# Optimization experiments

Hardware: AMD Instinct MI355X
Metric: run time of the kernel (lower is better)

## Reference

```python
import jax, jax.numpy as jnp
import numpy as np

NSTATES = 16
NCOM = 4
NHIDDEN = 256
BATCH = 262144


def _orthogonal(key, out_dim, in_dim):
    # mimic torch.nn.init.orthogonal_
    big, small = max(out_dim, in_dim), min(out_dim, in_dim)
    a = jax.random.normal(key, (big, small), dtype=jnp.float32)
    q, r = jnp.linalg.qr(a)
    q = q * jnp.sign(jnp.diagonal(r))  # make deterministic / uniform
    if out_dim < in_dim:
        q = q.T
    return q


def setup_inputs() -> dict:
    key = jax.random.key(0)
    k0, k1, k2, k3, k4 = jax.random.split(key, 5)
    zstates = jax.random.normal(k0, (BATCH, NSTATES), dtype=jnp.float32)
    W1 = _orthogonal(k1, NHIDDEN, NSTATES)            # lin1.weight [nhidden, nstates]
    W2 = _orthogonal(k2, NHIDDEN, NHIDDEN)            # lin2.weight
    W3 = _orthogonal(k3, NHIDDEN, NHIDDEN)            # lin3.weight
    W4 = _orthogonal(k4, NSTATES + NCOM, NHIDDEN)     # lin4.weight [nstates+ncom, nhidden]
    return {"zstates": zstates, "W1": W1, "W2": W2, "W3": W3, "W4": W4}


def _mlp(x, W1, W2, W3, W4):
    # torch Linear (no bias): y = x @ W.T
    h = jax.nn.log_sigmoid(x @ W1.T)
    h = h + jax.nn.log_sigmoid(h @ W2.T)
    h = h + jax.nn.log_sigmoid(h @ W3.T)
    return h @ W4.T


def reference(zstates, W1, W2, W3, W4):
    nstates = NSTATES

    def _get_com_dstates(s):  # s: [nstates]
        nnout = _mlp(s, W1, W2, W3, W4)
        dstates = nnout[:nstates]
        com = nnout[nstates:]
        return com, (dstates, com)

    jac_fcn = jax.vmap(jax.jacrev(_get_com_dstates, argnums=0, has_aux=True))
    dcom_jac, (dstates, com) = jac_fcn(zstates)   # dcom_jac: [B, ncom, nstates]
    # [B, nstates, ncom] concat dstates column -> [B, nstates, ncom+1]
    dcom_jac_t = jnp.swapaxes(dcom_jac, -2, -1)
    mat = jnp.concatenate([dcom_jac_t, dstates[..., None]], axis=-1)
    q, r = jnp.linalg.qr(mat)                     # reduced QR: q [B, nstates, ncom+1]
    dstates_ortho = q[..., -1] * r[..., -1, -1:]  # [B, nstates]
    return dstates_ortho
```

## Files before the change

### kernel.cpp

```cpp
#include <hip/hip_runtime.h>
#include <math.h>

#define NS 16
#define NC 4
#define NH 256
#define BATCH 262144
#define EPB 64
#define HSTR 264

typedef _Float16 half8 __attribute__((ext_vector_type(8)));
typedef _Float16 half4v __attribute__((ext_vector_type(4)));
typedef _Float16 half2v __attribute__((ext_vector_type(2)));
typedef float f32x4 __attribute__((ext_vector_type(4)));

#define MFMA16(a, b, c) __builtin_amdgcn_mfma_f32_16x16x32_f16((a), (b), (c), 0, 0, 0)

#define OFF_W2HI   0
#define OFF_W2LO   65536
#define OFF_W3HI   131072
#define OFF_W3LO   196608
#define OFF_W2THI  262144
#define OFF_W2TLO  327680
#define OFF_W3THI  393216
#define OFF_W3TLO  458752
#define OFF_W1PHI  524288
#define OFF_W1PLO  532480
#define OFF_W1THI  540672
#define OFF_W1TLO  544768
#define OFF_W4HI   548864
#define OFF_W4LO   552960
#define WS_HALVES  557056

__device__ __forceinline__ float logsigf(float a) {
    return fminf(a, 0.f) - __logf(1.f + __expf(-fabsf(a)));
}
__device__ __forceinline__ float siggf(float a) {
    return 1.f / (1.f + __expf(a));
}
__device__ __forceinline__ void split2(float x, _Float16& h, _Float16& l) {
    h = (_Float16)x;
    l = (_Float16)(x - (float)h);
}
__device__ __forceinline__ float wsum16(float v) {
    v += __shfl_xor(v, 1, 64);
    v += __shfl_xor(v, 2, 64);
    v += __shfl_xor(v, 4, 64);
    v += __shfl_xor(v, 8, 64);
    return v;
}
__device__ __forceinline__ unsigned h2u(half2v h) {
    union { half2v h; unsigned u; } c; c.h = h; return c.u;
}
__device__ __forceinline__ half2v u2h(unsigned u) {
    union { half2v h; unsigned u; } c; c.u = u; return c.h;
}
__device__ __forceinline__ uint2 packg(const float g[4]) {
    half2v a, b;
    a[0] = (_Float16)g[0]; a[1] = (_Float16)g[1];
    b[0] = (_Float16)g[2]; b[1] = (_Float16)g[3];
    return make_uint2(h2u(a), h2u(b));
}

extern "C" __global__ void __launch_bounds__(256)
prep_big(const float* __restrict__ W2, const float* __restrict__ W3,
         _Float16* __restrict__ ws) {
    const int mat = blockIdx.y;
    const float* W = mat ? W3 : W2;
    _Float16* Whi  = ws + (mat ? OFF_W3HI  : OFF_W2HI);
    _Float16* Wlo  = Whi + 65536;
    _Float16* WThi = ws + (mat ? OFF_W3THI : OFF_W2THI);
    _Float16* WTlo = WThi + 65536;
    const int r = blockIdx.x, c = threadIdx.x;
    float x = W[r * NH + c];
    _Float16 h, l; split2(x, h, l);
    Whi[r * NH + c] = h;  Wlo[r * NH + c] = l;
    WThi[c * NH + r] = h; WTlo[c * NH + r] = l;
}

extern "C" __global__ void __launch_bounds__(256)
prep_small(const float* __restrict__ W1, const float* __restrict__ W4,
           _Float16* __restrict__ ws) {
    _Float16* W1phi = ws + OFF_W1PHI;
    _Float16* W1plo = ws + OFF_W1PLO;
    _Float16* W1Thi = ws + OFF_W1THI;
    _Float16* W1Tlo = ws + OFF_W1TLO;
    _Float16* W4hi  = ws + OFF_W4HI;
    _Float16* W4lo  = ws + OFF_W4LO;
    const int t = threadIdx.x;
    #pragma unroll
    for (int s = 0; s < NS; s++) {
        float x = W1[t * NS + s];
        _Float16 h, l; split2(x, h, l);
        W1phi[t * 32 + s] = h;        W1plo[t * 32 + s] = l;
        W1phi[t * 32 + 16 + s] = (_Float16)0.f;
        W1plo[t * 32 + 16 + s] = (_Float16)0.f;
        W1Thi[s * NH + t] = h;        W1Tlo[s * NH + t] = l;
    }
    #pragma unroll
    for (int q = 0; q < 16; q++) {
        int idx = q * 256 + t;
        float x = W4[idx];
        _Float16 h, l; split2(x, h, l);
        W4hi[idx] = h; W4lo[idx] = l;
    }
}


__device__ __forceinline__ void gemm_fwd1(const _Float16* __restrict__ Ahi,
                                          const _Float16* U,
                                          int w, int lo16, int hi4, f32x4 acc[2][4]) {
    #pragma unroll
    for (int ks = 0; ks < 8; ks++) {
        half8 bh[4];
        #pragma unroll
        for (int n = 0; n < 4; n++)
            bh[n] = *(const half8*)&U[(16 * n + lo16) * HSTR + ks * 32 + hi4 * 8];
        #pragma unroll
        for (int m = 0; m < 2; m++) {
            int woff = (32 * w + 16 * m + lo16) * NH + ks * 32 + hi4 * 8;
            half8 ah = *(const half8*)&Ahi[woff];
            #pragma unroll
            for (int n = 0; n < 4; n++)
                acc[m][n] = MFMA16(ah, bh[n], acc[m][n]);
        }
    }
}

__device__ __forceinline__ void gemm_bwd1(const _Float16* __restrict__ Ahi,
                                          const _Float16* U,
                                          int w, int lo16, int hi4, f32x4 acc[2][8]) {
    #pragma unroll
    for (int ks = 0; ks < 8; ks++) {
        half8 bh[8];
        #pragma unroll
        for (int n = 0; n < 8; n++)
            bh[n] = *(const half8*)&U[(16 * n + lo16) * HSTR + ks * 32 + hi4 * 8];
        #pragma unroll
        for (int m = 0; m < 2; m++) {
            int woff = (32 * w + 16 * m + lo16) * NH + ks * 32 + hi4 * 8;
            half8 ah = *(const half8*)&Ahi[woff];
            #pragma unroll
            for (int n = 0; n < 8; n++)
                acc[m][n] = MFMA16(ah, bh[n], acc[m][n]);
        }
    }
}

__global__ void __launch_bounds__(512, 1)
comet_mfma(const float* __restrict__ Z,
           const float* __restrict__ W4,
           const _Float16* __restrict__ ws,
           float* __restrict__ OUT)
{
    const _Float16* W2hi  = ws + OFF_W2HI;
    const _Float16* W3hi  = ws + OFF_W3HI;
    const _Float16* W2Thi = ws + OFF_W2THI;
    const _Float16* W3Thi = ws + OFF_W3THI;
    const _Float16* W1phi = ws + OFF_W1PHI;
    const _Float16* W1plo = ws + OFF_W1PLO;
    const _Float16* W1Thi = ws + OFF_W1THI;
    const _Float16* W4hi  = ws + OFF_W4HI;
    const _Float16* W4lo  = ws + OFF_W4LO;

    __shared__ __align__(16) _Float16 U[128 * HSTR];
    __shared__ __align__(16) float Jfin[16 * 260];
    __shared__ __align__(16) float Pb[8 * 272];

    const int tid  = threadIdx.x;
    const int l    = tid & 63, w = tid >> 6;
    const int lo16 = l & 15, hi4 = l >> 4;
    const int ebase = blockIdx.x * EPB;
    const int c4 = lo16 & 3;

    float4 vreg[2];
    #pragma unroll
    for (int m = 0; m < 2; m++)
        vreg[m] = *(const float4*)&W4[(NS + c4) * NH + 32 * w + 16 * m + 4 * hi4];

    uint2 g1u[2][4], g2u[2][4], g3u[2][4];

    {
        f32x4 acc[2][4];
        #pragma unroll
        for (int m = 0; m < 2; m++)
            #pragma unroll
            for (int n = 0; n < 4; n++) acc[m][n] = (f32x4)(0.f);
        half8 bh[4], bl[4];
        #pragma unroll
        for (int n = 0; n < 4; n++) {
            if (hi4 < 2) {
                const float* zp = &Z[(size_t)(ebase + 16 * n + lo16) * NS + hi4 * 8];
                float4 z0 = *(const float4*)zp;
                float4 z1 = *(const float4*)(zp + 4);
                float zz[8] = {z0.x, z0.y, z0.z, z0.w, z1.x, z1.y, z1.z, z1.w};
                #pragma unroll
                for (int r = 0; r < 8; r++) {
                    _Float16 h, lo; split2(zz[r], h, lo);
                    bh[n][r] = h; bl[n][r] = lo;
                }
            } else {
                #pragma unroll
                for (int r = 0; r < 8; r++) { bh[n][r] = (_Float16)0.f; bl[n][r] = (_Float16)0.f; }
            }
        }
        #pragma unroll
        for (int m = 0; m < 2; m++) {
            int woff = (32 * w + 16 * m + lo16) * 32 + hi4 * 8;
            half8 ah = *(const half8*)&W1phi[woff];
            half8 al = *(const half8*)&W1plo[woff];
            #pragma unroll
            for (int n = 0; n < 4; n++) {
                acc[m][n] = MFMA16(ah, bh[n], acc[m][n]);
                acc[m][n] = MFMA16(al, bh[n], acc[m][n]);
                acc[m][n] = MFMA16(ah, bl[n], acc[m][n]);
            }
        }
        #pragma unroll
        for (int m = 0; m < 2; m++)
            #pragma unroll
            for (int n = 0; n < 4; n++) {
                int hoff = (16 * n + lo16) * HSTR + 32 * w + 16 * m + 4 * hi4;
                float gv[4];
                half4v nh, nl;
                #pragma unroll
                for (int r = 0; r < 4; r++) {
                    float a = acc[m][n][r];
                    gv[r] = siggf(a);
                    float hv = logsigf(a);
                    _Float16 xh, xl; split2(hv, xh, xl);
                    nh[r] = xh; nl[r] = xl;
                }
                g1u[m][n] = packg(gv);
                *(half4v*)&U[hoff] = nh;
                *(half4v*)&U[64 * HSTR + hoff] = nl;
            }
    }
    __syncthreads();

    #pragma unroll
    for (int L = 0; L < 2; L++) {
        f32x4 acc[2][4];
        #pragma unroll
        for (int m = 0; m < 2; m++)
            #pragma unroll
            for (int n = 0; n < 4; n++) acc[m][n] = (f32x4)(0.f);
        gemm_fwd1(L ? W3hi : W2hi, U, w, lo16, hi4, acc);
        __syncthreads();
        #pragma unroll
        for (int m = 0; m < 2; m++)
            #pragma unroll
            for (int n = 0; n < 4; n++) {
                int hoff = (16 * n + lo16) * HSTR + 32 * w + 16 * m + 4 * hi4;
                half4v oh = *(const half4v*)&U[hoff];
                half4v ol = *(const half4v*)&U[64 * HSTR + hoff];
                float gv[4];
                half4v nh, nl;
                #pragma unroll
                for (int r = 0; r < 4; r++) {
                    float a = acc[m][n][r];
                    gv[r] = siggf(a);
                    float hv = (float)oh[r] + (float)ol[r] + logsigf(a);
                    _Float16 xh, xl; split2(hv, xh, xl);
                    nh[r] = xh; nl[r] = xl;
                }
                if (L) g3u[m][n] = packg(gv); else g2u[m][n] = packg(gv);
                *(half4v*)&U[hoff] = nh;
                *(half4v*)&U[64 * HSTR + hoff] = nl;
            }
        __syncthreads();
    }

    {
        const int et = w & 3, kh = w >> 2;
        f32x4 acc = (f32x4)(0.f);
        #pragma unroll
        for (int i = 0; i < 4; i++) {
            int ks = 4 * kh + i;
            int boff = (16 * et + lo16) * HSTR + ks * 32 + hi4 * 8;
            half8 bh = *(const half8*)&U[boff];
            half8 bl = *(const half8*)&U[64 * HSTR + boff];
            int woff = lo16 * NH + ks * 32 + hi4 * 8;
            half8 ah = *(const half8*)&W4hi[woff];
            half8 al = *(const half8*)&W4lo[woff];
            acc = MFMA16(ah, bh, acc);
            acc = MFMA16(al, bh, acc);
            acc = MFMA16(ah, bl, acc);
        }
        #pragma unroll
        for (int r = 0; r < 4; r++)
            Pb[w * 272 + (hi4 * 4 + r) * 17 + lo16] = acc[r];
    }
    __syncthreads();

    #pragma unroll
    for (int p = 0; p < 2; p++) {
        #pragma unroll
        for (int m = 0; m < 2; m++)
            #pragma unroll
            for (int n = 0; n < 8; n++) {
                const int src = (l & 48) | (4 * (n & 3) + (lo16 >> 2));
                const int et = 2 * p + (n >> 2);
                const int kbase = 32 * w + 16 * m + 4 * hi4;
                unsigned ux = (unsigned)__shfl((int)g3u[m][et].x, src, 64);
                unsigned uy = (unsigned)__shfl((int)g3u[m][et].y, src, 64);
                half2v h0 = u2h(ux), h1 = u2h(uy);
                float g[4] = {(float)h0[0], (float)h0[1], (float)h1[0], (float)h1[1]};
                half4v vh;
                #pragma unroll
                for (int r = 0; r < 4; r++)
                    vh[r] = (_Float16)(vreg[m][r] * g[r]);
                *(half4v*)&U[(16 * n + lo16) * HSTR + kbase] = vh;
            }
        __syncthreads();

        f32x4 acc2[2][8];
        #pragma unroll
        for (int m = 0; m < 2; m++)
            #pragma unroll
            for (int n = 0; n < 8; n++) acc2[m][n] = (f32x4)(0.f);
        gemm_bwd1(W3Thi, U, w, lo16, hi4, acc2);
        __syncthreads();

        #pragma unroll
        for (int m = 0; m < 2; m++)
            #pragma unroll
            for (int n = 0; n < 8; n++) {
                const int src = (l & 48) | (4 * (n & 3) + (lo16 >> 2));
                const int et = 2 * p + (n >> 2);
                const int kbase = 32 * w + 16 * m + 4 * hi4;
                unsigned ux = (unsigned)__shfl((int)g2u[m][et].x, src, 64);
                unsigned uy = (unsigned)__shfl((int)g2u[m][et].y, src, 64);
                half2v h0 = u2h(ux), h1 = u2h(uy);
                float g[4] = {(float)h0[0], (float)h0[1], (float)h1[0], (float)h1[1]};
                half4v vh;
                #pragma unroll
                for (int r = 0; r < 4; r++) {
                    float gg2 = vreg[m][r] + acc2[m][n][r];
                    acc2[m][n][r] = gg2;
                    vh[r] = (_Float16)(gg2 * g[r]);
                }
                *(half4v*)&U[(16 * n + lo16) * HSTR + kbase] = vh;
            }
        __syncthreads();

        gemm_bwd1(W2Thi, U, w, lo16, hi4, acc2);
        __syncthreads();

        #pragma unroll
        for (int m = 0; m < 2; m++)
            #pragma unroll
            for (int n = 0; n < 8; n++) {
                const int src = (l & 48) | (4 * (n & 3) + (lo16 >> 2));
                const int et = 2 * p + (n >> 2);
                const int kbase = 32 * w + 16 * m + 4 * hi4;
                unsigned ux = (unsigned)__shfl((int)g1u[m][et].x, src, 64);
                unsigned uy = (unsigned)__shfl((int)g1u[m][et].y, src, 64);
                half2v h0 = u2h(ux), h1 = u2h(uy);
                float g[4] = {(float)h0[0], (float)h0[1], (float)h1[0], (float)h1[1]};
                half4v vh;
                #pragma unroll
                for (int r = 0; r < 4; r++)
                    vh[r] = (_Float16)(acc2[m][n][r] * g[r]);
                *(half4v*)&U[(16 * n + lo16) * HSTR + kbase] = vh;
            }
        __syncthreads();

        {
            f32x4 accj = (f32x4)(0.f);
            #pragma unroll
            for (int ks = 0; ks < 8; ks++) {
                int boff = (16 * w + lo16) * HSTR + ks * 32 + hi4 * 8;
                half8 bh = *(const half8*)&U[boff];
                int woff = lo16 * NH + ks * 32 + hi4 * 8;
                half8 ah = *(const half8*)&W1Thi[woff];
                accj = MFMA16(ah, bh, accj);
            }
            #pragma unroll
            for (int r = 0; r < 4; r++)
                Jfin[(4 * hi4 + r) * 260 + 128 * p + 16 * w + lo16] = accj[r];
        }
        __syncthreads();
    }

    #pragma unroll
    for (int half = 0; half < 2; half++) {
        const int e = 8 * w + 4 * half + hi4, s = lo16;
        float acol[4];
        #pragma unroll
        for (int c = 0; c < 4; c++) acol[c] = Jfin[s * 260 + 4 * e + c];
        const int et = e >> 4, c16 = e & 15;
        float dval = Pb[et * 272 + s * 17 + c16] + Pb[(et + 4) * 272 + s * 17 + c16];
        #pragma unroll
        for (int c = 0; c < 4; c++) {
            float n2 = wsum16(acol[c] * acol[c]);
            float inv = (n2 > 1e-30f) ? (1.0f / sqrtf(n2)) : 0.0f;
            float q = acol[c] * inv;
            #pragma unroll
            for (int cc = c + 1; cc < 4; cc++) {
                float pj = wsum16(acol[cc] * q);
                acol[cc] -= pj * q;
            }
            float pd = wsum16(dval * q);
            dval -= pd * q;
        }
        OUT[(size_t)(ebase + e) * NS + s] = dval;
    }
}

__device__ __forceinline__ float dot4f(float4 a, float4 b) {
    return a.x*b.x + a.y*b.y + a.z*b.z + a.w*b.w;
}

__global__ void __launch_bounds__(256, 2)
comet_fused_f32(const float* __restrict__ Z,
                const float* __restrict__ W1,
                const float* __restrict__ W2,
                const float* __restrict__ W3,
                const float* __restrict__ W4,
                float* __restrict__ OUT)
{
    __shared__ __align__(16) float h_lds[4][4][NH];
    __shared__ __align__(16) float m_lds[4][4][NH][NC];

    const int l = threadIdx.x & 63;
    const int w = threadIdx.x >> 6;
    float (*hb)[NH]     = h_lds[w];
    float (*mb)[NH][NC] = m_lds[w];
    const int ebase = (blockIdx.x * 4 + w) * 4;

    float d1g[4][4], d2g[4][4], d3g[4][4];

    {
        float acc[4][4];
        #pragma unroll
        for (int j = 0; j < 4; j++)
            #pragma unroll
            for (int e = 0; e < 4; e++) acc[j][e] = 0.f;
        #pragma unroll
        for (int s4 = 0; s4 < 4; s4++) {
            float4 wf[4];
            #pragma unroll
            for (int j = 0; j < 4; j++)
                wf[j] = *(const float4*)&W1[(l + 64*j) * NS + s4*4];
            #pragma unroll
            for (int e = 0; e < 4; e++) {
                float4 xv = *(const float4*)&Z[(ebase + e) * NS + s4*4];
                #pragma unroll
                for (int j = 0; j < 4; j++) acc[j][e] += dot4f(wf[j], xv);
            }
        }
        #pragma unroll
        for (int j = 0; j < 4; j++)
            #pragma unroll
            for (int e = 0; e < 4; e++) {
                float a = acc[j][e];
                d1g[j][e] = siggf(a);
                hb[e][l + 64*j] = logsigf(a);
            }
    }
    __syncthreads();

#define FWD_LAYER(WPTR, GARR)                                                   \
    {                                                                           \
        float acc[4][4];                                                        \
        _Pragma("unroll")                                                       \
        for (int j = 0; j < 4; j++) {                                           \
            _Pragma("unroll")                                                   \
            for (int e = 0; e < 4; e++) acc[j][e] = 0.f;                        \
        }                                                                       \
        _Pragma("unroll 2")                                                     \
        for (int kk = 0; kk < NH; kk += 4) {                                    \
            float wv[4][4];                                                     \
            _Pragma("unroll")                                                   \
            for (int j = 0; j < 4; j++) {                                       \
                float4 t = *(const float4*)&WPTR[(l + 64*j) * NH + kk];         \
                wv[0][j] = t.x; wv[1][j] = t.y; wv[2][j] = t.z; wv[3][j] = t.w; \
            }                                                                   \
            _Pragma("unroll")                                                   \
            for (int e = 0; e < 4; e++) {                                       \
                float4 hv = *(const float4*)&hb[e][kk];                         \
                _Pragma("unroll")                                               \
                for (int j = 0; j < 4; j++)                                     \
                    acc[j][e] += wv[0][j]*hv.x + wv[1][j]*hv.y                  \
                               + wv[2][j]*hv.z + wv[3][j]*hv.w;                 \
            }                                                                   \
        }                                                                       \
        __syncthreads();                                                        \
        _Pragma("unroll")                                                       \
        for (int j = 0; j < 4; j++) {                                           \
            _Pragma("unroll")                                                   \
            for (int e = 0; e < 4; e++) {                                       \
                float a = acc[j][e];                                            \
                GARR[j][e] = siggf(a);                                          \
                hb[e][l + 64*j] += logsigf(a);                                  \
            }                                                                   \
        }                                                                       \
        __syncthreads();                                                        \
    }

    FWD_LAYER(W2, d2g)
    FWD_LAYER(W3, d3g)
#undef FWD_LAYER

    const int e4 = l >> 4, s4 = l & 15;
    float dval = 0.f;
    {
        #pragma unroll 2
        for (int kk = 0; kk < NH; kk += 4) {
            float4 wf = *(const float4*)&W4[s4 * NH + kk];
            float4 hv = *(const float4*)&hb[e4][kk];
            dval += dot4f(wf, hv);
        }
    }

    float gacc[4][4][4];
    float vf[4][4];
    #pragma unroll
    for (int c = 0; c < 4; c++)
        #pragma unroll
        for (int j = 0; j < 4; j++)
            vf[c][j] = W4[(NS + c) * NH + l + 64*j];
    #pragma unroll
    for (int e = 0; e < 4; e++)
        #pragma unroll
        for (int c = 0; c < 4; c++)
            #pragma unroll
            for (int j = 0; j < 4; j++)
                gacc[e][c][j] = vf[c][j];
    #pragma unroll
    for (int j = 0; j < 4; j++)
        #pragma unroll
        for (int e = 0; e < 4; e++) {
            float g = d3g[j][e];
            float4 mv = make_float4(vf[0][j]*g, vf[1][j]*g, vf[2][j]*g, vf[3][j]*g);
            *(float4*)&mb[e][l + 64*j][0] = mv;
        }
    __syncthreads();

#define BWD_GEMM(WPTR)                                                          \
    {                                                                           \
        _Pragma("unroll 2")                                                     \
        for (int r = 0; r < NH; r++) {                                          \
            float wc[4];                                                        \
            _Pragma("unroll")                                                   \
            for (int j = 0; j < 4; j++) wc[j] = WPTR[r * NH + l + 64*j];        \
            _Pragma("unroll")                                                   \
            for (int e = 0; e < 4; e++) {                                       \
                float4 mv = *(const float4*)&mb[e][r][0];                       \
                _Pragma("unroll")                                               \
                for (int j = 0; j < 4; j++) {                                   \
                    gacc[e][0][j] += wc[j]*mv.x;                                \
                    gacc[e][1][j] += wc[j]*mv.y;                                \
                    gacc[e][2][j] += wc[j]*mv.z;                                \
                    gacc[e][3][j] += wc[j]*mv.w;                                \
                }                                                               \
            }                                                                   \
        }                                                                       \
    }

    BWD_GEMM(W3)
    __syncthreads();
    #pragma unroll
    for (int j = 0; j < 4; j++)
        #pragma unroll
        for (int e = 0; e < 4; e++) {
            float g = d2g[j][e];
            float4 mv = make_float4(gacc[e][0][j]*g, gacc[e][1][j]*g,
                                    gacc[e][2][j]*g, gacc[e][3][j]*g);
            *(float4*)&mb[e][l + 64*j][0] = mv;
        }
    __syncthreads();
    BWD_GEMM(W2)
#undef BWD_GEMM
    __syncthreads();
    #pragma unroll
    for (int j = 0; j < 4; j++)
        #pragma unroll
        for (int e = 0; e < 4; e++) {
            float g = d1g[j][e];
            float4 mv = make_float4(gacc[e][0][j]*g, gacc[e][1][j]*g,
                                    gacc[e][2][j]*g, gacc[e][3][j]*g);
            *(float4*)&mb[e][l + 64*j][0] = mv;
        }
    __syncthreads();

    const int c4 = l >> 4;
    float jv[4] = {0.f, 0.f, 0.f, 0.f};
    #pragma unroll 4
    for (int r = 0; r < NH; r++) {
        float w1v = W1[r * NS + s4];
        #pragma unroll
        for (int e = 0; e < 4; e++) jv[e] += mb[e][r][c4] * w1v;
    }
    __syncthreads();

    float* jlds = (float*)hb;
    #pragma unroll
    for (int e = 0; e < 4; e++) jlds[e * 64 + c4 * 16 + s4] = jv[e];
    __syncthreads();

    float acol[4];
    acol[0] = jlds[e4 * 64 +      s4];
    acol[1] = jlds[e4 * 64 + 16 + s4];
    acol[2] = jlds[e4 * 64 + 32 + s4];
    acol[3] = jlds[e4 * 64 + 48 + s4];
    #pragma unroll
    for (int c = 0; c < 4; c++) {
        float n2 = wsum16(acol[c] * acol[c]);
        float inv = (n2 > 1e-30f) ? (1.0f / sqrtf(n2)) : 0.0f;
        float q = acol[c] * inv;
        #pragma unroll
        for (int cc = c + 1; cc < 4; cc++) {
            float p = wsum16(acol[cc] * q);
            acol[cc] -= p * q;
        }
        float pd = wsum16(dval * q);
        dval -= pd * q;
    }
    OUT[ebase * NS + l] = dval;
}

extern "C" void kernel_launch(void* const* d_in, const int* in_sizes, int n_in,
                              void* d_out, int out_size, void* d_ws, size_t ws_size,
                              hipStream_t stream) {
    const float* Z  = (const float*)d_in[0];
    const float* W1 = (const float*)d_in[1];
    const float* W2 = (const float*)d_in[2];
    const float* W3 = (const float*)d_in[3];
    const float* W4 = (const float*)d_in[4];
    float* OUT = (float*)d_out;

    const size_t need = (size_t)WS_HALVES * sizeof(_Float16);

    if (ws_size >= need) {
        _Float16* ws = (_Float16*)d_ws;
        hipLaunchKernelGGL(prep_big, dim3(NH, 2), dim3(NH), 0, stream, W2, W3, ws);
        hipLaunchKernelGGL(prep_small, dim3(1), dim3(NH), 0, stream, W1, W4, ws);
        hipLaunchKernelGGL(comet_mfma, dim3(BATCH / EPB), dim3(512), 0, stream,
                           Z, W4, ws, OUT);
    } else {
        hipLaunchKernelGGL(comet_fused_f32, dim3(BATCH / 16), dim3(256), 0, stream,
                           Z, W1, W2, W3, W4, OUT);
    }
}
```

Baseline: 891.6 us.

## Drop lo-half activation split, fuse sigmoid/logsigmoid, use packed fp16 gating

Forward hidden activations are now stored only as a single fp16 copy instead of a hi/lo split pair. This removes the lo LDS writes and reads and one of the three MFMAs per step in the W4 projection. Sigmoid and log-sigmoid now share one exp and a hardware reciprocal, and the backward gating multiplies are done as packed fp16 pairs using pkrtz conversion. The cost is lower precision in the forward state and in the Jacobian inputs, which could hurt the accuracy of the QR-based output.

```diff
diff --git a/kernel.cpp b/kernel.cpp
--- a/kernel.cpp
+++ b/kernel.cpp
@@ -37,6 +37,13 @@
 __device__ __forceinline__ float siggf(float a) {
     return 1.f / (1.f + __expf(a));
 }
+__device__ __forceinline__ void act2(float a, float& ls, float& g) {
+    float e  = __expf(-fabsf(a));
+    float om = 1.f + e;
+    float r  = __builtin_amdgcn_rcpf(om);
+    ls = fminf(a, 0.f) - __logf(om);
+    g  = (a >= 0.f) ? e * r : r;
+}
 __device__ __forceinline__ void split2(float x, _Float16& h, _Float16& l) {
     h = (_Float16)x;
     l = (_Float16)(x - (float)h);
@@ -54,12 +61,14 @@
 __device__ __forceinline__ half2v u2h(unsigned u) {
     union { half2v h; unsigned u; } c; c.u = u; return c.h;
 }
-__device__ __forceinline__ uint2 packg(const float g[4]) {
-    half2v a, b;
-    a[0] = (_Float16)g[0]; a[1] = (_Float16)g[1];
-    b[0] = (_Float16)g[2]; b[1] = (_Float16)g[3];
-    return make_uint2(h2u(a), h2u(b));
-}
+__device__ __forceinline__ half2v pkrtz(float a, float b) {
+    auto t = __builtin_amdgcn_cvt_pkrtz(a, b);
+    union { decltype(t) s; half2v d; } c; c.s = t; return c.d;
+}
+__device__ __forceinline__ uint2 packg2(float g0, float g1, float g2, float g3) {
+    return make_uint2(h2u(pkrtz(g0, g1)), h2u(pkrtz(g2, g3)));
+}
+union H4u { half4v v4; half2v v2[2]; };
 
 extern "C" __global__ void __launch_bounds__(256)
 prep_big(const float* __restrict__ W2, const float* __restrict__ W3,
@@ -173,9 +182,13 @@
     const int c4 = lo16 & 3;
 
     float4 vreg[2];
-    #pragma unroll
-    for (int m = 0; m < 2; m++)
+    half2v vregh[2][2];
+    #pragma unroll
+    for (int m = 0; m < 2; m++) {
         vreg[m] = *(const float4*)&W4[(NS + c4) * NH + 32 * w + 16 * m + 4 * hi4];
+        vregh[m][0] = pkrtz(vreg[m].x, vreg[m].y);
+        vregh[m][1] = pkrtz(vreg[m].z, vreg[m].w);
+    }
 
     uint2 g1u[2][4], g2u[2][4], g3u[2][4];
 
@@ -221,18 +234,16 @@
             for (int n = 0; n < 4; n++) {
                 int hoff = (16 * n + lo16) * HSTR + 32 * w + 16 * m + 4 * hi4;
                 float gv[4];
-                half4v nh, nl;
+                half4v nh;
                 #pragma unroll
                 for (int r = 0; r < 4; r++) {
-                    float a = acc[m][n][r];
-                    gv[r] = siggf(a);
-                    float hv = logsigf(a);
-                    _Float16 xh, xl; split2(hv, xh, xl);
-                    nh[r] = xh; nl[r] = xl;
+                    float ls, g;
+                    act2(acc[m][n][r], ls, g);
+                    gv[r] = g;
+                    nh[r] = (_Float16)ls;
                 }
-                g1u[m][n] = packg(gv);
+                g1u[m][n] = packg2(gv[0], gv[1], gv[2], gv[3]);
                 *(half4v*)&U[hoff] = nh;
-                *(half4v*)&U[64 * HSTR + hoff] = nl;
             }
     }
     __syncthreads();
@@ -252,20 +263,18 @@
             for (int n = 0; n < 4; n++) {
                 int hoff = (16 * n + lo16) * HSTR + 32 * w + 16 * m + 4 * hi4;
                 half4v oh = *(const half4v*)&U[hoff];
-                half4v ol = *(const half4v*)&U[64 * HSTR + hoff];
                 float gv[4];
-                half4v nh, nl;
+                half4v nh;
                 #pragma unroll
                 for (int r = 0; r < 4; r++) {
-                    float a = acc[m][n][r];
-                    gv[r] = siggf(a);
-                    float hv = (float)oh[r] + (float)ol[r] + logsigf(a);
-                    _Float16 xh, xl; split2(hv, xh, xl);
-                    nh[r] = xh; nl[r] = xl;
+                    float ls, g;
+                    act2(acc[m][n][r], ls, g);
+                    gv[r] = g;
+                    nh[r] = (_Float16)((float)oh[r] + ls);
                 }
-                if (L) g3u[m][n] = packg(gv); else g2u[m][n] = packg(gv);
+                if (L) g3u[m][n] = packg2(gv[0], gv[1], gv[2], gv[3]);
+                else   g2u[m][n] = packg2(gv[0], gv[1], gv[2], gv[3]);
                 *(half4v*)&U[hoff] = nh;
-                *(half4v*)&U[64 * HSTR + hoff] = nl;
             }
         __syncthreads();
     }
@@ -278,13 +287,11 @@
             int ks = 4 * kh + i;
             int boff = (16 * et + lo16) * HSTR + ks * 32 + hi4 * 8;
             half8 bh = *(const half8*)&U[boff];
-            half8 bl = *(const half8*)&U[64 * HSTR + boff];
             int woff = lo16 * NH + ks * 32 + hi4 * 8;
             half8 ah = *(const half8*)&W4hi[woff];
             half8 al = *(const half8*)&W4lo[woff];
             acc = MFMA16(ah, bh, acc);
             acc = MFMA16(al, bh, acc);
-            acc = MFMA16(ah, bl, acc);
         }
         #pragma unroll
         for (int r = 0; r < 4; r++)
@@ -301,15 +308,12 @@
                 const int src = (l & 48) | (4 * (n & 3) + (lo16 >> 2));
                 const int et = 2 * p + (n >> 2);
                 const int kbase = 32 * w + 16 * m + 4 * hi4;
-                unsigned ux = (unsigned)__shfl((int)g3u[m][et].x, src, 64);
-                unsigned uy = (unsigned)__shfl((int)g3u[m][et].y, src, 64);
-                half2v h0 = u2h(ux), h1 = u2h(uy);
-                float g[4] = {(float)h0[0], (float)h0[1], (float)h1[0], (float)h1[1]};
-                half4v vh;
-                #pragma unroll
-                for (int r = 0; r < 4; r++)
-                    vh[r] = (_Float16)(vreg[m][r] * g[r]);
-                *(half4v*)&U[(16 * n + lo16) * HSTR + kbase] = vh;
+                half2v g01 = u2h((unsigned)__shfl((int)g3u[m][et].x, src, 64));
+                half2v g23 = u2h((unsigned)__shfl((int)g3u[m][et].y, src, 64));
+                H4u t;
+                t.v2[0] = vregh[m][0] * g01;
+                t.v2[1] = vregh[m][1] * g23;
+                *(half4v*)&U[(16 * n + lo16) * HSTR + kbase] = t.v4;
             }
         __syncthreads();
 
@@ -328,18 +332,18 @@
                 const int src = (l & 48) | (4 * (n & 3) + (lo16 >> 2));
                 const int et = 2 * p + (n >> 2);
                 const int kbase = 32 * w + 16 * m + 4 * hi4;
-                unsigned ux = (unsigned)__shfl((int)g2u[m][et].x, src, 64);
-                unsigned uy = (unsigned)__shfl((int)g2u[m][et].y, src, 64);
-                half2v h0 = u2h(ux), h1 = u2h(uy);
-                float g[4] = {(float)h0[0], (float)h0[1], (float)h1[0], (float)h1[1]};
-                half4v vh;
+                half2v g01 = u2h((unsigned)__shfl((int)g2u[m][et].x, src, 64));
+                half2v g23 = u2h((unsigned)__shfl((int)g2u[m][et].y, src, 64));
+                float gg[4];
                 #pragma unroll
                 for (int r = 0; r < 4; r++) {
-                    float gg2 = vreg[m][r] + acc2[m][n][r];
-                    acc2[m][n][r] = gg2;
-                    vh[r] = (_Float16)(gg2 * g[r]);
+                    gg[r] = vreg[m][r] + acc2[m][n][r];
+                    acc2[m][n][r] = gg[r];
                 }
-                *(half4v*)&U[(16 * n + lo16) * HSTR + kbase] = vh;
+                H4u t;
+                t.v2[0] = pkrtz(gg[0], gg[1]) * g01;
+                t.v2[1] = pkrtz(gg[2], gg[3]) * g23;
+                *(half4v*)&U[(16 * n + lo16) * HSTR + kbase] = t.v4;
             }
         __syncthreads();
 
@@ -353,15 +357,12 @@
                 const int src = (l & 48) | (4 * (n & 3) + (lo16 >> 2));
                 const int et = 2 * p + (n >> 2);
                 const int kbase = 32 * w + 16 * m + 4 * hi4;
-                unsigned ux = (unsigned)__shfl((int)g1u[m][et].x, src, 64);
-                unsigned uy = (unsigned)__shfl((int)g1u[m][et].y, src, 64);
-                half2v h0 = u2h(ux), h1 = u2h(uy);
-                float g[4] = {(float)h0[0], (float)h0[1], (float)h1[0], (float)h1[1]};
-                half4v vh;
-                #pragma unroll
-                for (int r = 0; r < 4; r++)
-                    vh[r] = (_Float16)(acc2[m][n][r] * g[r]);
-                *(half4v*)&U[(16 * n + lo16) * HSTR + kbase] = vh;
+                half2v g01 = u2h((unsigned)__shfl((int)g1u[m][et].x, src, 64));
+                half2v g23 = u2h((unsigned)__shfl((int)g1u[m][et].y, src, 64));
+                H4u t;
+                t.v2[0] = pkrtz(acc2[m][n][0], acc2[m][n][1]) * g01;
+                t.v2[1] = pkrtz(acc2[m][n][2], acc2[m][n][3]) * g23;
+                *(half4v*)&U[(16 * n + lo16) * HSTR + kbase] = t.v4;
             }
         __syncthreads();
 
```

Result: faster. 796.4 us (-10.7%).
